# Kernel optimization log

Hardware: AMD Instinct MI355X
Metric: run time of the kernel (lower is better)

Reference implementation:

```python
import jax, jax.numpy as jnp
import numpy as np

NODES = 163842
IN_FEATS = 32
OUT_FEATS = 64

def setup_inputs() -> dict:
    key = jax.random.key(0)
    k1, k2, k3, k4, k5 = jax.random.split(key, 5)
    x = jax.random.normal(k1, (NODES, IN_FEATS), dtype=jnp.float32)
    # 0-based neighbor indices (original stores 1-based and subtracts 1)
    neigh_indices = jax.random.randint(k2, (NODES, 25, 3), 0, NODES, dtype=jnp.int32)
    # barycentric interpolation weights per (node, 25 template positions, 3 triangle verts)
    neigh_weights = jax.random.uniform(k3, (NODES, 25, 3), dtype=jnp.float32)
    W = jax.random.normal(k4, (OUT_FEATS, 25 * IN_FEATS), dtype=jnp.float32) * 0.02
    b = jax.random.normal(k5, (OUT_FEATS,), dtype=jnp.float32) * 0.02
    return {"x": x, "neigh_indices": neigh_indices, "neigh_weights": neigh_weights, "W": W, "b": b}

def reference(x, neigh_indices, neigh_weights, W, b):
    nodes, c = x.shape
    # gather neighbor features: (nodes, 25, 3, in_feats)
    mat = x[neigh_indices.reshape(-1)].reshape(nodes, 25, 3, c)
    # barycentric weighted sum over the 3 triangle vertices -> (nodes, 25, in_feats)
    feat = jnp.sum(mat * neigh_weights[..., None], axis=2)
    # flatten the 25 template positions and project: (nodes, out_feats)
    feat = feat.reshape(nodes, 25 * c)
    return feat @ W.T + b
```

## Files before the change

kernel.cpp:

```cpp
#include <hip/hip_runtime.h>
#include <hip/hip_bf16.h>

#define NNODES   163842
#define INF      32
#define OUTF     64
#define NPOS     25
#define KTOT     800
#define MT       64
#define NTHREADS 256

typedef float  f32x4  __attribute__((ext_vector_type(4)));
typedef __bf16 bf16x8 __attribute__((ext_vector_type(8)));
typedef __bf16 bf16x4 __attribute__((ext_vector_type(4)));

__global__ void cvt_kernel(const float* __restrict__ x, const float* __restrict__ W,
                           __bf16* __restrict__ xb, __bf16* __restrict__ wb) {
    int tid = blockIdx.x * blockDim.x + threadIdx.x;
    int stride = gridDim.x * blockDim.x;
    const f32x4* x4 = (const f32x4*)x;
    bf16x4* xb4 = (bf16x4*)xb;
    const int nx4 = NNODES * INF / 4;
    for (int j = tid; j < nx4; j += stride) {
        f32x4 v = x4[j];
        bf16x4 o;
        #pragma unroll
        for (int k = 0; k < 4; ++k) o[k] = (__bf16)v[k];
        xb4[j] = o;
    }
    const f32x4* w4 = (const f32x4*)W;
    bf16x4* wb4 = (bf16x4*)wb;
    const int nw4 = OUTF * KTOT / 4;
    for (int j = tid; j < nw4; j += stride) {
        f32x4 v = w4[j];
        bf16x4 o;
        #pragma unroll
        for (int k = 0; k < 4; ++k) o[k] = (__bf16)v[k];
        wb4[j] = o;
    }
}

__launch_bounds__(NTHREADS)
__global__ void conv_mfma(const int* __restrict__ nidx, const float* __restrict__ nwt,
                          const __bf16* __restrict__ xb, const __bf16* __restrict__ wb,
                          const float* __restrict__ bias, float* __restrict__ out) {
    __shared__ int   idxs[MT * 75];
    __shared__ float wts [MT * 75];
    __shared__ __align__(16) __bf16 feat[MT][48];

    const int tid  = threadIdx.x;
    const int base = blockIdx.x * MT;

    {
        const long gbase = (long)base * 75;
        const long tot   = (long)NNODES * 75;
        for (int i = tid; i < MT * 75; i += NTHREADS) {
            long g = gbase + i;
            if (g < tot) { idxs[i] = nidx[g]; wts[i] = nwt[g]; }
            else         { idxs[i] = 0;       wts[i] = 0.0f;  }
        }
    }

    const int lane = tid & 63;
    const int wave = tid >> 6;
    const int gn = tid >> 2;
    const int gc = (tid & 3) * 8;
    const int arow = lane & 15;
    const int kgrp = lane >> 4;

    f32x4 acc[4] = {{0,0,0,0},{0,0,0,0},{0,0,0,0},{0,0,0,0}};

    __syncthreads();

    for (int p = 0; p < NPOS; ++p) {
        {
            const int ib = gn * 75 + p * 3;
            const int i0 = idxs[ib+0], i1 = idxs[ib+1], i2 = idxs[ib+2];
            const float w0 = wts[ib+0], w1 = wts[ib+1], w2 = wts[ib+2];
            bf16x8 v0 = *(const bf16x8*)(xb + i0 * INF + gc);
            bf16x8 v1 = *(const bf16x8*)(xb + i1 * INF + gc);
            bf16x8 v2 = *(const bf16x8*)(xb + i2 * INF + gc);
            bf16x8 fv;
            #pragma unroll
            for (int j = 0; j < 8; ++j) {
                float f = w0 * (float)v0[j] + w1 * (float)v1[j] + w2 * (float)v2[j];
                fv[j] = (__bf16)f;
            }
            *(bf16x8*)(&feat[gn][gc]) = fv;
        }
        __syncthreads();
        {
            bf16x8 afrag = *(const bf16x8*)(&feat[16*wave + arow][8*kgrp]);
            const int koff = p * 32 + 8 * kgrp;
            #pragma unroll
            for (int nb = 0; nb < 4; ++nb) {
                bf16x8 bfrag = *(const bf16x8*)(wb + (16*nb + arow) * KTOT + koff);
                acc[nb] = __builtin_amdgcn_mfma_f32_16x16x32_bf16(afrag, bfrag, acc[nb], 0, 0, 0);
            }
        }
        __syncthreads();
    }

    #pragma unroll
    for (int nb = 0; nb < 4; ++nb) {
        const int col = 16*nb + arow;
        const float bv = bias[col];
        #pragma unroll
        for (int r = 0; r < 4; ++r) {
            const int row = base + 16*wave + 4*kgrp + r;
            if (row < NNODES) out[(long)row * OUTF + col] = acc[nb][r] + bv;
        }
    }
}

__global__ void conv_fallback(const float* __restrict__ x, const int* __restrict__ nidx,
                              const float* __restrict__ nwt, const float* __restrict__ W,
                              const float* __restrict__ bias, float* __restrict__ out) {
    __shared__ float feat[KTOT];
    const int n = blockIdx.x;
    const int t = threadIdx.x;
    for (int e = t; e < KTOT; e += 64) {
        const int p = e >> 5, c = e & 31;
        const int ib = n * 75 + p * 3;
        float a = 0.0f;
        #pragma unroll
        for (int v = 0; v < 3; ++v)
            a += nwt[ib+v] * x[nidx[ib+v] * INF + c];
        feat[e] = a;
    }
    __syncthreads();
    float a = bias[t];
    const float* wr = W + t * KTOT;
    for (int k = 0; k < KTOT; ++k) a += feat[k] * wr[k];
    out[(long)n * OUTF + t] = a;
}

extern "C" void kernel_launch(void* const* d_in, const int* in_sizes, int n_in,
                              void* d_out, int out_size, void* d_ws, size_t ws_size,
                              hipStream_t stream) {
    const float* x    = (const float*)d_in[0];
    const int*   nidx = (const int*)  d_in[1];
    const float* nwt  = (const float*)d_in[2];
    const float* W    = (const float*)d_in[3];
    const float* bias = (const float*)d_in[4];
    float* out = (float*)d_out;

    const size_t need = (size_t)NNODES * INF * 2 + (size_t)OUTF * KTOT * 2;
    if (ws_size < need) {
        conv_fallback<<<NNODES, 64, 0, stream>>>(x, nidx, nwt, W, bias, out);
        return;
    }

    __bf16* xb = (__bf16*)d_ws;
    __bf16* wb = xb + (size_t)NNODES * INF;

    cvt_kernel<<<1024, NTHREADS, 0, stream>>>(x, W, xb, wb);
    const int nblocks = (NNODES + MT - 1) / MT;
    conv_mfma<<<nblocks, NTHREADS, 0, stream>>>(nidx, nwt, xb, wb, bias, out);
}
```

Baseline: 203.0 us.

## Drop LDS staging and barriers; compute MFMA A-fragments in registers with prefetched indices

Removes the shared-memory staging of indices, weights and the feature tile, along with the per-position __syncthreads. Each lane now gathers its own node's neighbor rows and builds the MFMA A-fragment directly in registers. Positions are processed in groups of five, and the next group's indices are loaded before the current group is processed so gather latency overlaps. The goal is to cut barrier stalls and LDS traffic and to expose more memory-level parallelism, at the cost of higher register pressure and uncoalesced per-lane index and weight loads.

```diff
diff --git a/kernel.cpp b/kernel.cpp
--- a/kernel.cpp
+++ b/kernel.cpp
@@ -43,62 +43,61 @@
 __global__ void conv_mfma(const int* __restrict__ nidx, const float* __restrict__ nwt,
                           const __bf16* __restrict__ xb, const __bf16* __restrict__ wb,
                           const float* __restrict__ bias, float* __restrict__ out) {
-    __shared__ int   idxs[MT * 75];
-    __shared__ float wts [MT * 75];
-    __shared__ __align__(16) __bf16 feat[MT][48];
-
     const int tid  = threadIdx.x;
-    const int base = blockIdx.x * MT;
-
-    {
-        const long gbase = (long)base * 75;
-        const long tot   = (long)NNODES * 75;
-        for (int i = tid; i < MT * 75; i += NTHREADS) {
-            long g = gbase + i;
-            if (g < tot) { idxs[i] = nidx[g]; wts[i] = nwt[g]; }
-            else         { idxs[i] = 0;       wts[i] = 0.0f;  }
-        }
-    }
-
     const int lane = tid & 63;
     const int wave = tid >> 6;
-    const int gn = tid >> 2;
-    const int gc = (tid & 3) * 8;
     const int arow = lane & 15;
     const int kgrp = lane >> 4;
+    const int gc   = kgrp * 8;
+    const int base = blockIdx.x * MT + wave * 16;
+    const int node = min(base + arow, NNODES - 1);
+    const long ibase = (long)node * 75;
 
     f32x4 acc[4] = {{0,0,0,0},{0,0,0,0},{0,0,0,0},{0,0,0,0}};
 
-    __syncthreads();
+    int ia[15], ib[15];
 
-    for (int p = 0; p < NPOS; ++p) {
-        {
-            const int ib = gn * 75 + p * 3;
-            const int i0 = idxs[ib+0], i1 = idxs[ib+1], i2 = idxs[ib+2];
-            const float w0 = wts[ib+0], w1 = wts[ib+1], w2 = wts[ib+2];
-            bf16x8 v0 = *(const bf16x8*)(xb + i0 * INF + gc);
-            bf16x8 v1 = *(const bf16x8*)(xb + i1 * INF + gc);
-            bf16x8 v2 = *(const bf16x8*)(xb + i2 * INF + gc);
-            bf16x8 fv;
+    auto loadidx = [&](int g, int (&ii)[15]) {
+        #pragma unroll
+        for (int i = 0; i < 15; ++i) ii[i] = nidx[ibase + g * 15 + i];
+    };
+
+    auto dogroup = [&](int g, const int (&ii)[15]) {
+        bf16x8 v[15];
+        float  w[15];
+        #pragma unroll
+        for (int t = 0; t < 15; ++t)
+            v[t] = *(const bf16x8*)(xb + (long)ii[t] * INF + gc);
+        #pragma unroll
+        for (int t = 0; t < 15; ++t)
+            w[t] = nwt[ibase + g * 15 + t];
+        #pragma unroll
+        for (int p = 0; p < 5; ++p) {
+            bf16x8 af;
             #pragma unroll
-            for (int j = 0; j < 8; ++j) {
-                float f = w0 * (float)v0[j] + w1 * (float)v1[j] + w2 * (float)v2[j];
-                fv[j] = (__bf16)f;
-            }
-            *(bf16x8*)(&feat[gn][gc]) = fv;
-        }
-        __syncthreads();
-        {
-            bf16x8 afrag = *(const bf16x8*)(&feat[16*wave + arow][8*kgrp]);
-            const int koff = p * 32 + 8 * kgrp;
+            for (int j = 0; j < 8; ++j)
+                af[j] = (__bf16)(w[p*3+0] * (float)v[p*3+0][j]
+                               + w[p*3+1] * (float)v[p*3+1][j]
+                               + w[p*3+2] * (float)v[p*3+2][j]);
+            const int koff = (g * 5 + p) * INF + gc;
             #pragma unroll
             for (int nb = 0; nb < 4; ++nb) {
-                bf16x8 bfrag = *(const bf16x8*)(wb + (16*nb + arow) * KTOT + koff);
-                acc[nb] = __builtin_amdgcn_mfma_f32_16x16x32_bf16(afrag, bfrag, acc[nb], 0, 0, 0);
+                bf16x8 bw = *(const bf16x8*)(wb + (16*nb + arow) * KTOT + koff);
+                acc[nb] = __builtin_amdgcn_mfma_f32_16x16x32_bf16(af, bw, acc[nb], 0, 0, 0);
             }
         }
-        __syncthreads();
-    }
+    };
+
+    loadidx(0, ia);
+    loadidx(1, ib);
+    dogroup(0, ia);
+    loadidx(2, ia);
+    dogroup(1, ib);
+    loadidx(3, ib);
+    dogroup(2, ia);
+    loadidx(4, ia);
+    dogroup(3, ib);
+    dogroup(4, ia);
 
     #pragma unroll
     for (int nb = 0; nb < 4; ++nb) {
@@ -106,7 +105,7 @@
         const float bv = bias[col];
         #pragma unroll
         for (int r = 0; r < 4; ++r) {
-            const int row = base + 16*wave + 4*kgrp + r;
+            const int row = base + 4*kgrp + r;
             if (row < NNODES) out[(long)row * OUTF + col] = acc[nb][r] + bv;
         }
     }
```

Result: slower. 225.2 us (+10.9%).
